# Performance work log

Measured on AMD Instinct MI355X. Metric: run time of the kernel, lower is better.

Reference implementation:

```python
import jax, jax.numpy as jnp
import numpy as np

N_NODES = 100000
N_EDGES = 400000  # per edge type
N_ETYPES = 3
N_LAYERS = 3      # 1 + (n_layers-1) + 1 with n_layers=2
D = 64


def setup_inputs() -> dict:
    key = jax.random.key(0)
    k1, k2, k3, k4, k5 = jax.random.split(key, 5)
    feat = jax.random.normal(k1, (N_NODES, D), dtype=jnp.float32)
    # SAGEConv weights per (layer, etype): fc_self, fc_neigh, bias
    W_self = jax.random.normal(k2, (N_LAYERS, N_ETYPES, D, D), dtype=jnp.float32) * 0.05
    W_neigh = jax.random.normal(k3, (N_LAYERS, N_ETYPES, D, D), dtype=jnp.float32) * 0.05
    b = jnp.zeros((N_LAYERS, N_ETYPES, D), dtype=jnp.float32)
    src = jax.random.randint(k4, (N_ETYPES, N_EDGES), 0, N_NODES, dtype=jnp.int32)
    dst = jax.random.randint(k5, (N_ETYPES, N_EDGES), 0, N_NODES, dtype=jnp.int32)
    return {"feat": feat, "W_self": W_self, "W_neigh": W_neigh, "b": b,
            "src": src, "dst": dst}


def reference(feat, W_self, W_neigh, b, src, dst):
    # Heterogeneous SAGEConv (mean aggregator) + cross-relation sum, 3 layers.
    N = feat.shape[0]
    L, T = W_self.shape[0], W_self.shape[1]
    E = src.shape[1]
    ones = jnp.ones((E,), dtype=feat.dtype)
    h = feat
    for l in range(L):
        apply_act = l < L - 1  # last layer has no activation
        out = jnp.zeros((N, W_self.shape[-1]), dtype=feat.dtype)
        for t in range(T):  # small fixed set of relation types
            msgs = jnp.take(h, src[t], axis=0)                    # [E, d] gather
            agg = jax.ops.segment_sum(msgs, dst[t], num_segments=N)   # [N, d]
            deg = jax.ops.segment_sum(ones, dst[t], num_segments=N)   # [N]
            mean = agg / jnp.maximum(deg, 1.0)[:, None]           # zero-deg -> 0
            r = h @ W_self[l, t] + mean @ W_neigh[l, t] + b[l, t]
            if apply_act:
                r = jax.nn.relu(r)
            out = out + r  # HeteroGraphConv aggregate='sum'
        h = out
    return h
```

## Files before the change

kernel.cpp:

```cpp
#include <hip/hip_runtime.h>
#include <hip/hip_bf16.h>

#define NN 100000
#define NE 400000
#define NT 3
#define NL 3
#define DD 64
#define M_TOT (NT * NN)
#define RPB 2048
#define NBKT ((M_TOT + RPB - 1) / RPB)
#define P3CAP 64
#define P3GRID 512
#define PCAP 16384
#define CSR_THREADS 1024
#define COLCAP_BKT 9216
#define OVF_CAP 500000


typedef __attribute__((ext_vector_type(8))) short bf16x8;
typedef __attribute__((ext_vector_type(4))) float f32x4;

static __device__ __forceinline__ unsigned short f2b(float f) {
    __hip_bfloat16 b = __float2bfloat16(f);
    return *reinterpret_cast<unsigned short*>(&b);
}
static __device__ __forceinline__ float b2f(unsigned short u) {
    __hip_bfloat16 b = *reinterpret_cast<__hip_bfloat16*>(&u);
    return __bfloat162float(b);
}

__global__ __launch_bounds__(256) void pair_scatter(
    const int* __restrict__ src, const int* __restrict__ dst,
    int* __restrict__ gcur, unsigned* __restrict__ pairs,
    uint2* __restrict__ ovf, int* __restrict__ ocnt) {
    __shared__ unsigned buf[NBKT][P3CAP];
    __shared__ int fill[NBKT];
    for (int i = threadIdx.x; i < NBKT; i += 256) fill[i] = 0;
    __syncthreads();
    const int total = NT * NE;
    int per = (total + gridDim.x - 1) / gridDim.x;
    int beg = blockIdx.x * per;
    int fin = beg + per; if (fin > total) fin = total;
    for (int bse = beg; bse < fin; bse += 512) {
#pragma unroll
        for (int half = 0; half < 2; ++half) {
            int e = bse + half * 256 + threadIdx.x;
            if (e < fin) {
                int t = e / NE;
                int row = t * NN + dst[e];
                int bk = row >> 11;
                unsigned pr = ((unsigned)(row & 2047) << 17) | (unsigned)src[e];
                int pos = atomicAdd(&fill[bk], 1);
                if (pos < P3CAP) buf[bk][pos] = pr;
                else {
                    int o = atomicAdd(ocnt, 1);
                    if (o < OVF_CAP)
                        ovf[o] = make_uint2((unsigned)src[e], (unsigned)row);
                }
            }
        }
        __syncthreads();
        for (int bk = threadIdx.x; bk < NBKT; bk += 256) {
            int n = fill[bk]; if (n > P3CAP) n = P3CAP;
            int g = n >> 4;
            if (g) {
                int gb = atomicAdd(&gcur[bk], g * 16);
                for (int grp = 0; grp < g; ++grp)
#pragma unroll
                    for (int q = 0; q < 4; ++q)
                        *(int4*)&pairs[gb + grp * 16 + q * 4] =
                            *(const int4*)&buf[bk][grp * 16 + q * 4];
                int rem = n - g * 16;
                for (int k = 0; k < rem; ++k) buf[bk][k] = buf[bk][g * 16 + k];
                fill[bk] = rem;
            } else fill[bk] = n;
        }
        __syncthreads();
    }
    for (int bk = threadIdx.x; bk < NBKT; bk += 256) {
        int n = fill[bk]; if (n > P3CAP) n = P3CAP;
        if (n) {
            int m = (n + 15) & ~15;
            for (int k = n; k < m; ++k) buf[bk][k] = 0xFFFFFFFFu;
            int gb = atomicAdd(&gcur[bk], m);
            for (int grp = 0; grp < m >> 4; ++grp)
#pragma unroll
                for (int q = 0; q < 4; ++q)
                    *(int4*)&pairs[gb + grp * 16 + q * 4] =
                        *(const int4*)&buf[bk][grp * 16 + q * 4];
        }
    }
}

__global__ __launch_bounds__(CSR_THREADS) void bucket_csr(
    const int* __restrict__ gcur, const unsigned* __restrict__ pairs,
    const uint2* __restrict__ ovf, const int* __restrict__ ocnt,
    int* __restrict__ rs, int* __restrict__ rse, int* __restrict__ col) {
    __shared__ int cnt_s[RPB];
    __shared__ int cur_s[RPB];
    __shared__ int part[CSR_THREADS];
    const int bk = blockIdx.x;
    const int row0 = bk * RPB;
    const int nrows = (M_TOT - row0 < RPB) ? (M_TOT - row0) : RPB;
    for (int i = threadIdx.x; i < RPB; i += CSR_THREADS) cnt_s[i] = 0;
    __syncthreads();
    const int pb = bk * PCAP, pe = gcur[bk];
    for (int p = pb + threadIdx.x; p < pe; p += CSR_THREADS) {
        unsigned pr = pairs[p];
        if ((pr & 0x1FFFFu) < NN)
            atomicAdd(&cnt_s[pr >> 17], 1);
    }
    int no = ocnt[0]; if (no > OVF_CAP) no = OVF_CAP;
    for (int o = threadIdx.x; o < no; o += CSR_THREADS) {
        int rl = (int)ovf[o].y - row0;
        if (rl >= 0 && rl < nrows) atomicAdd(&cnt_s[rl], 1);
    }
    __syncthreads();
    int t0 = threadIdx.x * 2, sum = 0;
    int exl[2];
#pragma unroll
    for (int k = 0; k < 2; ++k) { exl[k] = sum; sum += cnt_s[t0 + k]; }
    part[threadIdx.x] = sum;
    __syncthreads();
    for (int o = 1; o < CSR_THREADS; o <<= 1) {
        int v = (threadIdx.x >= o) ? part[threadIdx.x - o] : 0;
        __syncthreads();
        part[threadIdx.x] += v;
        __syncthreads();
    }
    int off = part[threadIdx.x] - sum + bk * COLCAP_BKT;
#pragma unroll
    for (int k = 0; k < 2; ++k) {
        int idx = t0 + k;
        int ex = exl[k] + off;
        cur_s[idx] = ex;
        if (idx < nrows) { rs[row0 + idx] = ex; rse[row0 + idx] = ex + cnt_s[idx]; }
    }
    __syncthreads();
    for (int p = pb + threadIdx.x; p < pe; p += CSR_THREADS) {
        unsigned pr = pairs[p];
        unsigned s = pr & 0x1FFFFu;
        if (s < NN) {
            int pos = atomicAdd(&cur_s[pr >> 17], 1);
            col[pos] = (int)s;
        }
    }
    for (int o = threadIdx.x; o < no; o += CSR_THREADS) {
        int rl = (int)ovf[o].y - row0;
        if (rl >= 0 && rl < nrows) {
            int pos = atomicAdd(&cur_s[rl], 1);
            col[pos] = (int)ovf[o].x;
        }
    }
}

__global__ __launch_bounds__(256) void wtrans_kernel(
    const float* __restrict__ Ws, const float* __restrict__ Wn,
    unsigned short* __restrict__ Wt, int* __restrict__ gcur,
    int* __restrict__ ocnt) {
    int lt = blockIdx.x;
    if (lt == 0) {
        int i = threadIdx.x;
        if (i < NBKT) gcur[i] = i * PCAP;
        if (i == 0) ocnt[0] = 0;
    }
    for (int p = threadIdx.x; p < DD * 2 * DD; p += 256) {
        int j = p >> 7, k = p & 127;
        float v = (k < DD) ? Ws[(size_t)lt * DD * DD + k * DD + j]
                           : Wn[(size_t)lt * DD * DD + (k - DD) * DD + j];
        Wt[(size_t)lt * 8192 + j * 128 + k] = f2b(v);
    }
}

template <int HBF>
__global__ __launch_bounds__(256) void gather_kernel(
    const void* __restrict__ hv, const int* __restrict__ rs,
    const int* __restrict__ rse, const int* __restrict__ col,
    unsigned short* __restrict__ meanb) {
    const int lane = threadIdx.x & 63;
    const int g = lane >> 3;
    const int fc = lane & 7;
    const int i = (blockIdx.x * 4 + (threadIdx.x >> 6)) * 8 + g;
    const bool live = i < M_TOT;
    const int start = live ? rs[i] : 0;
    const int end   = live ? rse[i] : 0;
    const int deg = end - start;
    float acc[8];
#pragma unroll
    for (int j = 0; j < 8; ++j) acc[j] = 0.f;
    const unsigned short* hb = (const unsigned short*)hv;
    const float* hf = (const float*)hv;
    for (int base = 0; base < deg; base += 8) {
        int e = start + base + fc;
        int cl = col[(e < end) ? e : start];

#define GSTEP(K)                                                               \
        {                                                                      \
            int idx = __builtin_amdgcn_ds_swizzle(cl, ((K) << 5) | 24);        \
            bool v = (base + (K)) < deg;                                       \
            float mk = v ? 1.f : 0.f;                                          \
            int ix = v ? idx : 0;                                              \
            if (HBF) {                                                         \
                int4 rv = *(const int4*)&hb[(size_t)ix * DD + fc * 8];         \
                const unsigned* wp = (const unsigned*)&rv;                     \
                _Pragma("unroll")                                              \
                for (int j = 0; j < 4; ++j) {                                  \
                    unsigned w = wp[j];                                        \
                    float lo = __uint_as_float(w << 16);                       \
                    float hi = __uint_as_float(w & 0xffff0000u);               \
                    acc[2 * j]     = fmaf(lo, mk, acc[2 * j]);                 \
                    acc[2 * j + 1] = fmaf(hi, mk, acc[2 * j + 1]);             \
                }                                                              \
            } else {                                                           \
                float4 a = *(const float4*)&hf[(size_t)ix * DD + fc * 8];      \
                float4 b = *(const float4*)&hf[(size_t)ix * DD + fc * 8 + 4];  \
                acc[0] = fmaf(a.x, mk, acc[0]);                                \
                acc[1] = fmaf(a.y, mk, acc[1]);                                \
                acc[2] = fmaf(a.z, mk, acc[2]);                                \
                acc[3] = fmaf(a.w, mk, acc[3]);                                \
                acc[4] = fmaf(b.x, mk, acc[4]);                                \
                acc[5] = fmaf(b.y, mk, acc[5]);                                \
                acc[6] = fmaf(b.z, mk, acc[6]);                                \
                acc[7] = fmaf(b.w, mk, acc[7]);                                \
            }                                                                  \
        }
        GSTEP(0) GSTEP(1) GSTEP(2) GSTEP(3)
        GSTEP(4) GSTEP(5) GSTEP(6) GSTEP(7)
#undef GSTEP
    }
    float sc = (deg > 0) ? 1.f / (float)deg : 0.f;
    unsigned ow[4];
#pragma unroll
    for (int j = 0; j < 4; ++j) {
        unsigned lo = f2b(acc[2 * j] * sc);
        unsigned hi = f2b(acc[2 * j + 1] * sc);
        ow[j] = lo | (hi << 16);
    }
    if (live)
        *(int4*)&meanb[(size_t)i * DD + fc * 8] = *(const int4*)ow;
}

template <int HBF, int OBF>
__global__ __launch_bounds__(256) void layer_gemm(
    const void* __restrict__ hv, const unsigned short* __restrict__ meanb,
    const unsigned short* __restrict__ Wt, const float* __restrict__ bias,
    void* __restrict__ outv, int relu) {
    __shared__ __align__(16) short A_s[64 * 136];
    __shared__ __align__(16) short B_s[64 * 136];

    const int tx = threadIdx.x;
    const int n0 = blockIdx.x * 64;
    const int lane = tx & 63, w = tx >> 6;
    const int q = lane >> 4, m16 = lane & 15;
    const int rr = tx >> 4;
    const int k0 = (tx & 15) * 4;
    const int bj = tx >> 2;
    const int bk = (tx & 3) * 32;

#pragma unroll
    for (int qq = 0; qq < 4; ++qq) {
        int r = rr + 16 * qq;
        int n = n0 + r;
        ushort4 hb4 = make_ushort4(0, 0, 0, 0);
        if (n < NN) {
            if (HBF) {
                hb4 = *(const ushort4*)&((const unsigned short*)hv)[(size_t)n * DD + k0];
            } else {
                float4 hf = *(const float4*)&((const float*)hv)[(size_t)n * DD + k0];
                hb4 = make_ushort4(f2b(hf.x), f2b(hf.y), f2b(hf.z), f2b(hf.w));
            }
        }
        *(ushort4*)&A_s[r * 136 + k0] = hb4;
    }

    float acc_sum[4][4];
#pragma unroll
    for (int c = 0; c < 4; ++c)
#pragma unroll
        for (int r = 0; r < 4; ++r) acc_sum[c][r] = 0.f;

    for (int t = 0; t < NT; ++t) {
#pragma unroll
        for (int qq = 0; qq < 4; ++qq) {
            int r = rr + 16 * qq;
            int n = n0 + r;
            ushort4 mv = make_ushort4(0, 0, 0, 0);
            if (n < NN)
                mv = *(const ushort4*)&meanb[((size_t)t * NN + n) * DD + k0];
            *(ushort4*)&A_s[r * 136 + 64 + k0] = mv;
        }
        {
            const unsigned short* wt = Wt + (size_t)t * 8192 + bj * 128 + bk;
#pragma unroll
            for (int u = 0; u < 4; ++u)
                *(int4*)&B_s[bj * 136 + bk + u * 8] = *(const int4*)&wt[u * 8];
        }
        __syncthreads();

        f32x4 acc[4];
#pragma unroll
        for (int c = 0; c < 4; ++c) acc[c] = (f32x4){0.f, 0.f, 0.f, 0.f};
#pragma unroll
        for (int kt = 0; kt < 4; ++kt) {
            bf16x8 a = *(const bf16x8*)&A_s[(16 * w + m16) * 136 + kt * 32 + q * 8];
#pragma unroll
            for (int c = 0; c < 4; ++c) {
                bf16x8 b = *(const bf16x8*)&B_s[(c * 16 + m16) * 136 + kt * 32 + q * 8];
                acc[c] = __builtin_amdgcn_mfma_f32_16x16x32_bf16(a, b, acc[c], 0, 0, 0);
            }
        }

#pragma unroll
        for (int c = 0; c < 4; ++c) {
            float bv = bias[t * DD + c * 16 + m16];
#pragma unroll
            for (int r = 0; r < 4; ++r) {
                float v = acc[c][r] + bv;
                if (relu) v = fmaxf(v, 0.f);
                acc_sum[c][r] += v;
            }
        }
        __syncthreads();
    }

#pragma unroll
    for (int c = 0; c < 4; ++c)
#pragma unroll
        for (int r = 0; r < 4; ++r) {
            int n = n0 + 16 * w + q * 4 + r;
            if (n >= NN) continue;
            size_t idx = (size_t)n * DD + c * 16 + m16;
            if (OBF)
                ((unsigned short*)outv)[idx] = f2b(acc_sum[c][r]);
            else
                ((float*)outv)[idx] = acc_sum[c][r];
        }
}

extern "C" void kernel_launch(void* const* d_in, const int* in_sizes, int n_in,
                              void* d_out, int out_size, void* d_ws, size_t ws_size,
                              hipStream_t stream) {
    const float* feat    = (const float*)d_in[0];
    const float* W_self  = (const float*)d_in[1];
    const float* W_neigh = (const float*)d_in[2];
    const float* bias    = (const float*)d_in[3];
    const int* src = (const int*)d_in[4];
    const int* dst = (const int*)d_in[5];

    char* ws = (char*)d_ws;
    int* gcur  = (int*)(ws + 0);
    int* ocnt  = (int*)(ws + 1024);
    int* rs    = (int*)(ws + 8192);
    int* rse   = (int*)(ws + 1208320);
    int* col   = (int*)(ws + 2408448);
    unsigned short* Wt    = (unsigned short*)(ws + 7827584);
    unsigned short* X2    = (unsigned short*)(ws + 7975040);
    unsigned short* meanb = (unsigned short*)(ws + 20775040);
    unsigned*       pairs = (unsigned*)(ws + 20775040);
    uint2*          ovf   = (uint2*)(ws + 20775040 + 12582912);

    wtrans_kernel<<<NL * NT, 256, 0, stream>>>(W_self, W_neigh, Wt, gcur, ocnt);
    pair_scatter<<<P3GRID, 256, 0, stream>>>(src, dst, gcur, pairs, ovf, ocnt);
    bucket_csr<<<NBKT, CSR_THREADS, 0, stream>>>(gcur, pairs, ovf, ocnt,
                                                 rs, rse, col);

    unsigned short* X1 = (unsigned short*)d_out;
    const int ggrid = (M_TOT + 31) / 32;
    const int mgrid = (NN + 63) / 64;

    gather_kernel<0><<<ggrid, 256, 0, stream>>>(feat, rs, rse, col, meanb);
    layer_gemm<0, 1><<<mgrid, 256, 0, stream>>>(
        feat, meanb, Wt + 0 * NT * 8192, bias + 0 * NT * DD, X1, 1);
    gather_kernel<1><<<ggrid, 256, 0, stream>>>(X1, rs, rse, col, meanb);
    layer_gemm<1, 1><<<mgrid, 256, 0, stream>>>(
        X1, meanb, Wt + 1 * NT * 8192, bias + 1 * NT * DD, X2, 1);
    gather_kernel<1><<<ggrid, 256, 0, stream>>>(X2, rs, rse, col, meanb);
    layer_gemm<1, 0><<<mgrid, 256, 0, stream>>>(
        X2, meanb, Wt + 2 * NT * 8192, bias + 2 * NT * DD, d_out, 0);
}
```

Measured before the change: 292.2 us.

## Fuse neighbor mean gather into per-layer MFMA GEMM kernel

Removes the separate gather kernel and its bf16 mean buffer in global memory. Each GEMM block now computes the mean aggregation for its 64 nodes per relation directly into shared memory before the MFMA step. It also halves the pair_scatter grid and shrinks the per-bucket pair capacity, moving the overflow region. The cost is fewer parallel blocks doing the irregular gather (about 1563 blocks versus about 9375), which may reduce latency hiding, and a smaller PCAP that could push more edges into the overflow path.

```diff
diff --git a/kernel.cpp b/kernel.cpp
--- a/kernel.cpp
+++ b/kernel.cpp
@@ -10,8 +10,8 @@
 #define RPB 2048
 #define NBKT ((M_TOT + RPB - 1) / RPB)
 #define P3CAP 64
-#define P3GRID 512
-#define PCAP 16384
+#define P3GRID 256
+#define PCAP 13312
 #define CSR_THREADS 1024
 #define COLCAP_BKT 9216
 #define OVF_CAP 500000
@@ -23,10 +23,6 @@
 static __device__ __forceinline__ unsigned short f2b(float f) {
     __hip_bfloat16 b = __float2bfloat16(f);
     return *reinterpret_cast<unsigned short*>(&b);
-}
-static __device__ __forceinline__ float b2f(unsigned short u) {
-    __hip_bfloat16 b = *reinterpret_cast<__hip_bfloat16*>(&u);
-    return __bfloat162float(b);
 }
 
 __global__ __launch_bounds__(256) void pair_scatter(
@@ -172,77 +168,10 @@
     }
 }
 
-template <int HBF>
-__global__ __launch_bounds__(256) void gather_kernel(
+template <int HBF, int OBF>
+__global__ __launch_bounds__(256) void layer_fused(
     const void* __restrict__ hv, const int* __restrict__ rs,
     const int* __restrict__ rse, const int* __restrict__ col,
-    unsigned short* __restrict__ meanb) {
-    const int lane = threadIdx.x & 63;
-    const int g = lane >> 3;
-    const int fc = lane & 7;
-    const int i = (blockIdx.x * 4 + (threadIdx.x >> 6)) * 8 + g;
-    const bool live = i < M_TOT;
-    const int start = live ? rs[i] : 0;
-    const int end   = live ? rse[i] : 0;
-    const int deg = end - start;
-    float acc[8];
-#pragma unroll
-    for (int j = 0; j < 8; ++j) acc[j] = 0.f;
-    const unsigned short* hb = (const unsigned short*)hv;
-    const float* hf = (const float*)hv;
-    for (int base = 0; base < deg; base += 8) {
-        int e = start + base + fc;
-        int cl = col[(e < end) ? e : start];
-
-#define GSTEP(K)                                                               \
-        {                                                                      \
-            int idx = __builtin_amdgcn_ds_swizzle(cl, ((K) << 5) | 24);        \
-            bool v = (base + (K)) < deg;                                       \
-            float mk = v ? 1.f : 0.f;                                          \
-            int ix = v ? idx : 0;                                              \
-            if (HBF) {                                                         \
-                int4 rv = *(const int4*)&hb[(size_t)ix * DD + fc * 8];         \
-                const unsigned* wp = (const unsigned*)&rv;                     \
-                _Pragma("unroll")                                              \
-                for (int j = 0; j < 4; ++j) {                                  \
-                    unsigned w = wp[j];                                        \
-                    float lo = __uint_as_float(w << 16);                       \
-                    float hi = __uint_as_float(w & 0xffff0000u);               \
-                    acc[2 * j]     = fmaf(lo, mk, acc[2 * j]);                 \
-                    acc[2 * j + 1] = fmaf(hi, mk, acc[2 * j + 1]);             \
-                }                                                              \
-            } else {                                                           \
-                float4 a = *(const float4*)&hf[(size_t)ix * DD + fc * 8];      \
-                float4 b = *(const float4*)&hf[(size_t)ix * DD + fc * 8 + 4];  \
-                acc[0] = fmaf(a.x, mk, acc[0]);                                \
-                acc[1] = fmaf(a.y, mk, acc[1]);                                \
-                acc[2] = fmaf(a.z, mk, acc[2]);                                \
-                acc[3] = fmaf(a.w, mk, acc[3]);                                \
-                acc[4] = fmaf(b.x, mk, acc[4]);                                \
-                acc[5] = fmaf(b.y, mk, acc[5]);                                \
-                acc[6] = fmaf(b.z, mk, acc[6]);                                \
-                acc[7] = fmaf(b.w, mk, acc[7]);                                \
-            }                                                                  \
-        }
-        GSTEP(0) GSTEP(1) GSTEP(2) GSTEP(3)
-        GSTEP(4) GSTEP(5) GSTEP(6) GSTEP(7)
-#undef GSTEP
-    }
-    float sc = (deg > 0) ? 1.f / (float)deg : 0.f;
-    unsigned ow[4];
-#pragma unroll
-    for (int j = 0; j < 4; ++j) {
-        unsigned lo = f2b(acc[2 * j] * sc);
-        unsigned hi = f2b(acc[2 * j + 1] * sc);
-        ow[j] = lo | (hi << 16);
-    }
-    if (live)
-        *(int4*)&meanb[(size_t)i * DD + fc * 8] = *(const int4*)ow;
-}
-
-template <int HBF, int OBF>
-__global__ __launch_bounds__(256) void layer_gemm(
-    const void* __restrict__ hv, const unsigned short* __restrict__ meanb,
     const unsigned short* __restrict__ Wt, const float* __restrict__ bias,
     void* __restrict__ outv, int relu) {
     __shared__ __align__(16) short A_s[64 * 136];
@@ -256,6 +185,11 @@
     const int k0 = (tx & 15) * 4;
     const int bj = tx >> 2;
     const int bk = (tx & 3) * 32;
+    const int g = lane >> 3;
+    const int fc = lane & 7;
+
+    const unsigned short* hb = (const unsigned short*)hv;
+    const float* hf = (const float*)hv;
 
 #pragma unroll
     for (int qq = 0; qq < 4; ++qq) {
@@ -264,10 +198,10 @@
         ushort4 hb4 = make_ushort4(0, 0, 0, 0);
         if (n < NN) {
             if (HBF) {
-                hb4 = *(const ushort4*)&((const unsigned short*)hv)[(size_t)n * DD + k0];
+                hb4 = *(const ushort4*)&hb[(size_t)n * DD + k0];
             } else {
-                float4 hf = *(const float4*)&((const float*)hv)[(size_t)n * DD + k0];
-                hb4 = make_ushort4(f2b(hf.x), f2b(hf.y), f2b(hf.z), f2b(hf.w));
+                float4 hfv = *(const float4*)&hf[(size_t)n * DD + k0];
+                hb4 = make_ushort4(f2b(hfv.x), f2b(hfv.y), f2b(hfv.z), f2b(hfv.w));
             }
         }
         *(ushort4*)&A_s[r * 136 + k0] = hb4;
@@ -281,14 +215,66 @@
 
     for (int t = 0; t < NT; ++t) {
 #pragma unroll
-        for (int qq = 0; qq < 4; ++qq) {
-            int r = rr + 16 * qq;
-            int n = n0 + r;
-            ushort4 mv = make_ushort4(0, 0, 0, 0);
-            if (n < NN)
-                mv = *(const ushort4*)&meanb[((size_t)t * NN + n) * DD + k0];
-            *(ushort4*)&A_s[r * 136 + 64 + k0] = mv;
-        }
+        for (int p = 0; p < 2; ++p) {
+            const int r = w * 16 + p * 8 + g;
+            const int n = n0 + r;
+            const bool live = n < NN;
+            const int i = t * NN + n;
+            const int start = live ? rs[i] : 0;
+            const int end   = live ? rse[i] : 0;
+            const int deg = end - start;
+            float acc[8];
+#pragma unroll
+            for (int j = 0; j < 8; ++j) acc[j] = 0.f;
+            for (int base = 0; base < deg; base += 8) {
+                int e = start + base + fc;
+                int cl = col[(e < end) ? e : start];
+
+#define GSTEP(K)                                                               \
+                {                                                              \
+                    int idx = __builtin_amdgcn_ds_swizzle(cl, ((K) << 5) | 24);\
+                    bool v = (base + (K)) < deg;                               \
+                    float mk = v ? 1.f : 0.f;                                  \
+                    int ix = v ? idx : 0;                                      \
+                    if (HBF) {                                                 \
+                        int4 rv = *(const int4*)&hb[(size_t)ix * DD + fc * 8]; \
+                        const unsigned* wp = (const unsigned*)&rv;             \
+                        _Pragma("unroll")                                      \
+                        for (int j = 0; j < 4; ++j) {                          \
+                            unsigned wv = wp[j];                               \
+                            float lo = __uint_as_float(wv << 16);              \
+                            float hi = __uint_as_float(wv & 0xffff0000u);      \
+                            acc[2 * j]     = fmaf(lo, mk, acc[2 * j]);         \
+                            acc[2 * j + 1] = fmaf(hi, mk, acc[2 * j + 1]);     \
+                        }                                                      \
+                    } else {                                                   \
+                        float4 a = *(const float4*)&hf[(size_t)ix * DD + fc * 8];\
+                        float4 b = *(const float4*)&hf[(size_t)ix * DD + fc * 8 + 4];\
+                        acc[0] = fmaf(a.x, mk, acc[0]);                        \
+                        acc[1] = fmaf(a.y, mk, acc[1]);                        \
+                        acc[2] = fmaf(a.z, mk, acc[2]);                        \
+                        acc[3] = fmaf(a.w, mk, acc[3]);                        \
+                        acc[4] = fmaf(b.x, mk, acc[4]);                        \
+                        acc[5] = fmaf(b.y, mk, acc[5]);                        \
+                        acc[6] = fmaf(b.z, mk, acc[6]);                        \
+                        acc[7] = fmaf(b.w, mk, acc[7]);                        \
+                    }                                                          \
+                }
+                GSTEP(0) GSTEP(1) GSTEP(2) GSTEP(3)
+                GSTEP(4) GSTEP(5) GSTEP(6) GSTEP(7)
+#undef GSTEP
+            }
+            float sc = (deg > 0) ? 1.f / (float)deg : 0.f;
+            unsigned ow[4];
+#pragma unroll
+            for (int j = 0; j < 4; ++j) {
+                unsigned lo = f2b(acc[2 * j] * sc);
+                unsigned hi = f2b(acc[2 * j + 1] * sc);
+                ow[j] = lo | (hi << 16);
+            }
+            *(int4*)&A_s[r * 136 + 64 + fc * 8] = *(const int4*)ow;
+        }
+
         {
             const unsigned short* wt = Wt + (size_t)t * 8192 + bj * 128 + bk;
 #pragma unroll
@@ -355,9 +341,8 @@
     int* col   = (int*)(ws + 2408448);
     unsigned short* Wt    = (unsigned short*)(ws + 7827584);
     unsigned short* X2    = (unsigned short*)(ws + 7975040);
-    unsigned short* meanb = (unsigned short*)(ws + 20775040);
     unsigned*       pairs = (unsigned*)(ws + 20775040);
-    uint2*          ovf   = (uint2*)(ws + 20775040 + 12582912);
+    uint2*          ovf   = (uint2*)(ws + 20775040 + 8388608);
 
     wtrans_kernel<<<NL * NT, 256, 0, stream>>>(W_self, W_neigh, Wt, gcur, ocnt);
     pair_scatter<<<P3GRID, 256, 0, stream>>>(src, dst, gcur, pairs, ovf, ocnt);
@@ -365,16 +350,12 @@
                                                  rs, rse, col);
 
     unsigned short* X1 = (unsigned short*)d_out;
-    const int ggrid = (M_TOT + 31) / 32;
     const int mgrid = (NN + 63) / 64;
 
-    gather_kernel<0><<<ggrid, 256, 0, stream>>>(feat, rs, rse, col, meanb);
-    layer_gemm<0, 1><<<mgrid, 256, 0, stream>>>(
-        feat, meanb, Wt + 0 * NT * 8192, bias + 0 * NT * DD, X1, 1);
-    gather_kernel<1><<<ggrid, 256, 0, stream>>>(X1, rs, rse, col, meanb);
-    layer_gemm<1, 1><<<mgrid, 256, 0, stream>>>(
-        X1, meanb, Wt + 1 * NT * 8192, bias + 1 * NT * DD, X2, 1);
-    gather_kernel<1><<<ggrid, 256, 0, stream>>>(X2, rs, rse, col, meanb);
-    layer_gemm<1, 0><<<mgrid, 256, 0, stream>>>(
-        X2, meanb, Wt + 2 * NT * 8192, bias + 2 * NT * DD, d_out, 0);
-}
+    layer_fused<0, 1><<<mgrid, 256, 0, stream>>>(
+        feat, rs, rse, col, Wt + 0 * NT * 8192, bias + 0 * NT * DD, X1, 1);
+    layer_fused<1, 1><<<mgrid, 256, 0, stream>>>(
+        X1, rs, rse, col, Wt + 1 * NT * 8192, bias + 1 * NT * DD, X2, 1);
+    layer_fused<1, 0><<<mgrid, 256, 0, stream>>>(
+        X2, rs, rse, col, Wt + 2 * NT * 8192, bias + 2 * NT * DD, d_out, 0);
+}
```

Result: no change. 292.4 us (+0.1%).
